# Kernel tuning notes

Hardware: AMD Instinct MI355X
Metric: run time of the kernel (lower is better)

## Reference

```python
import jax, jax.numpy as jnp
import numpy as np

T = 2048          # patch tokens (multiple of 128 -> flash padding is no-op)
D = 1280          # hidden_size
H = 16            # num_heads
HD = D // H       # 80 head_dim
HALF = HD // 2    # 40 rotary dim
FF = 3420         # intermediate_size
DEPTH = 4
MERGE = 4         # spatial_merge_size**2
OUT = 3584        # merger d_model
PATCH_IN = 1176   # 3*2*14*14
WIN = 64          # tokens per attention window
EPS = 1e-6
SCALE = 1.0 / float(np.sqrt(HD))


def setup_inputs() -> dict:
    key = jax.random.key(0)
    ks = iter(jax.random.split(key, 64))
    rn = lambda shape, s=0.02: jax.random.normal(next(ks), shape, jnp.float32) * s
    inp = {}
    inp["x"] = jax.random.normal(next(ks), (T, PATCH_IN), jnp.float32)
    inp["rotary_pos_emb"] = jax.random.uniform(next(ks), (T, HALF), jnp.float32) * 6.2832
    inp["cu_window_seqlens"] = jnp.arange(0, T + 1, WIN, dtype=jnp.int32)  # [33]
    inp["patch_w"] = rn((PATCH_IN, D))
    # per-block params, stacked on leading DEPTH axis for lax.scan
    inp["qkv_w"] = rn((DEPTH, D, 3 * D))
    inp["qkv_b"] = rn((DEPTH, 3 * D))
    inp["proj_w"] = rn((DEPTH, D, D))
    inp["proj_b"] = rn((DEPTH, D))
    inp["norm1_s"] = jnp.ones((DEPTH, D), jnp.float32)
    inp["norm2_s"] = jnp.ones((DEPTH, D), jnp.float32)
    inp["gate_w"] = rn((DEPTH, D, FF))
    inp["gate_b"] = rn((DEPTH, FF))
    inp["up_w"] = rn((DEPTH, D, FF))
    inp["up_b"] = rn((DEPTH, FF))
    inp["down_w"] = rn((DEPTH, FF, D))
    inp["down_b"] = rn((DEPTH, D))
    # patch merger
    inp["lnq_s"] = jnp.ones((D,), jnp.float32)
    inp["fc1_w"] = rn((MERGE * D, MERGE * D))
    inp["fc1_b"] = rn((MERGE * D,))
    inp["fc2_w"] = rn((MERGE * D, OUT))
    inp["fc2_b"] = rn((OUT,))
    return inp


def _rmsnorm(x, scale):
    return x * scale * jax.lax.rsqrt(jnp.mean(x * x, axis=-1, keepdims=True) + EPS)


def reference(x, rotary_pos_emb, cu_window_seqlens, patch_w, qkv_w, qkv_b,
              proj_w, proj_b, norm1_s, norm2_s, gate_w, gate_b, up_w, up_b,
              down_w, down_b, lnq_s, fc1_w, fc1_b, fc2_w, fc2_b):
    # patch embed: strided conv with kernel==stride is a plain matmul
    h = x @ patch_w  # [T, D]

    # windowed segment ids (generate_window_segment_ids); T % 128 == 0 -> no pad
    idx = jnp.arange(T, dtype=jnp.int32)
    seg = jnp.searchsorted(cu_window_seqlens[1:], idx, side='right') + 1
    mask = seg[:, None] == seg[None, :]  # [T, T] window attention mask

    cos = jnp.cos(rotary_pos_emb)  # [T, HALF]
    sin = jnp.sin(rotary_pos_emb)

    def rope(t):  # t: [T, H, HD]
        r, i = t[..., :HALF], t[..., HALF:]
        c, s = cos[:, None, :], sin[:, None, :]
        return jnp.concatenate([r * c - i * s, r * s + i * c], axis=-1)

    def block(h, p):
        qw, qb, pw, pb, n1, n2, gw, gb, uw, ub, dw, db = p
        n = _rmsnorm(h, n1)
        q, k, v = jnp.split(n @ qw + qb, 3, axis=-1)
        q = rope(q.reshape(T, H, HD))
        k = rope(k.reshape(T, H, HD))
        v = v.reshape(T, H, HD)
        scores = jnp.einsum('qhd,khd->hqk', q, k) * SCALE
        scores = jnp.where(mask[None], scores, -1e30)
        attn = jax.nn.softmax(scores, axis=-1)
        o = jnp.einsum('hqk,khd->qhd', attn, v).reshape(T, D)
        h = h + o @ pw + pb
        n = _rmsnorm(h, n2)
        h = h + (jax.nn.silu(n @ gw + gb) * (n @ uw + ub)) @ dw + db
        return h, None

    h, _ = jax.lax.scan(block, h, (qkv_w, qkv_b, proj_w, proj_b, norm1_s,
                                   norm2_s, gate_w, gate_b, up_w, up_b,
                                   down_w, down_b))

    # patch merger: RMSNorm -> merge 2x2 spatial patches -> MLP
    m = _rmsnorm(h, lnq_s).reshape(-1, MERGE * D)  # [T//4, 5120]
    m = jax.nn.gelu(m @ fc1_w + fc1_b, approximate=False)
    return m @ fc2_w + fc2_b  # [T//4, OUT]
```

## Files before the change

### kernel.cpp

```cpp
#include <hip/hip_runtime.h>
#include <hip/hip_bf16.h>
#include <cstdint>
#include <cstddef>
#include <math.h>

#define T_TOK 2048
#define DMODEL 1280
#define NHEAD 16
#define HDIM 80
#define HALFD 40
#define FFDIM 3420
#define FF_PAD 3456
#define FFK_PAD 3424
#define PATCH_INDIM 1176
#define PATCHK_PAD 1184
#define DEPTH_L 4
#define OUTD 3584
#define WIN 64
#define NWIN (T_TOK / WIN)
#define MERGED 5120
#define EPSV 1e-6f
#define SCALE_ATTN 0.11180339887498949f

typedef __attribute__((ext_vector_type(8))) short short8;
typedef __attribute__((ext_vector_type(4))) float f32x4;
typedef unsigned short ushort_t;

template<int BN>
__global__ __launch_bounds__(256) void gemm_bf16(
    const ushort_t* __restrict__ A, const ushort_t* __restrict__ Bt,
    const float* __restrict__ bias, const float* __restrict__ res,
    float* __restrict__ C, int M, int Nreal, int Nc, int Kp)
{
    constexpr int MI = (BN == 128) ? 4 : 2;
    __shared__ ushort_t As[3][128 * 32];
    __shared__ ushort_t Bs[3][BN * 32];

    const int tid  = threadIdx.x;
    const int lane = tid & 63;
    const int wave = tid >> 6;

    const int row0 = blockIdx.y * 128;
    const int col0 = blockIdx.x * BN;
    const int wm0  = (BN == 128) ? (wave & 1) * 64 : wave * 32;
    const int wn0  = (BN == 128) ? (wave >> 1) * 64 : 0;

    f32x4 acc[MI][4] = {};

    const int ldr = tid >> 2;
    const int ldc = ((tid & 3) ^ (ldr & 3)) * 8;

    const int mrow = lane & 15;
    const int kswz = ((lane >> 4) ^ (mrow & 3)) * 8;
    const int nt   = Kp >> 5;

    auto stage = [&](int buf, int kk) {
        const ushort_t* ga = A  + (size_t)(row0 + ldr) * Kp + kk + ldc;
        __builtin_amdgcn_global_load_lds(
            (const __attribute__((address_space(1))) void*)ga,
            (__attribute__((address_space(3))) void*)(&As[buf][tid * 8]), 16, 0, 0);
        __builtin_amdgcn_global_load_lds(
            (const __attribute__((address_space(1))) void*)(ga + (size_t)64 * Kp),
            (__attribute__((address_space(3))) void*)(&As[buf][2048 + tid * 8]), 16, 0, 0);
        const ushort_t* gb = Bt + (size_t)(col0 + ldr) * Kp + kk + ldc;
        __builtin_amdgcn_global_load_lds(
            (const __attribute__((address_space(1))) void*)gb,
            (__attribute__((address_space(3))) void*)(&Bs[buf][tid * 8]), 16, 0, 0);
        if constexpr (BN == 128) {
            __builtin_amdgcn_global_load_lds(
                (const __attribute__((address_space(1))) void*)(gb + (size_t)64 * Kp),
                (__attribute__((address_space(3))) void*)(&Bs[buf][2048 + tid * 8]), 16, 0, 0);
        }
    };

    stage(0, 0);
    if (nt > 1) stage(1, 32);

    int cur = 0;
    for (int t = 0; t < nt; ++t) {
        if (t + 1 < nt) {
            if constexpr (BN == 128) asm volatile("s_waitcnt vmcnt(4)" ::: "memory");
            else                     asm volatile("s_waitcnt vmcnt(3)" ::: "memory");
        } else {
            asm volatile("s_waitcnt vmcnt(0)" ::: "memory");
        }
        __builtin_amdgcn_s_barrier();

        short8 af[MI], bf[4];
        #pragma unroll
        for (int i = 0; i < MI; i++)
            af[i] = *(const short8*)&As[cur][(wm0 + i * 16 + mrow) * 32 + kswz];
        #pragma unroll
        for (int j = 0; j < 4; j++)
            bf[j] = *(const short8*)&Bs[cur][(wn0 + j * 16 + mrow) * 32 + kswz];

        __builtin_amdgcn_s_setprio(1);
        #pragma unroll
        for (int i = 0; i < MI; i++)
            #pragma unroll
            for (int j = 0; j < 4; j++)
                acc[i][j] = __builtin_amdgcn_mfma_f32_16x16x32_bf16(
                    af[i], bf[j], acc[i][j], 0, 0, 0);
        __builtin_amdgcn_s_setprio(0);

        if (t + 2 < nt) {
            int pf = cur + 2; if (pf >= 3) pf -= 3;
            stage(pf, (t + 2) * 32);
        }
        cur = (cur == 2) ? 0 : cur + 1;
    }

    const int crow0 = row0 + wm0 + (lane >> 4) * 4;
    const int ccol0 = col0 + wn0 + (lane & 15);
    #pragma unroll
    for (int j = 0; j < 4; j++) {
        const int col = ccol0 + j * 16;
        if (col >= Nreal) continue;
        const float bv = bias ? bias[col] : 0.f;
        #pragma unroll
        for (int i = 0; i < MI; i++) {
            #pragma unroll
            for (int r = 0; r < 4; r++) {
                const int row = crow0 + i * 16 + r;
                float v = acc[i][j][r] + bv;
                if (res) v += res[(size_t)row * Nc + col];
                C[(size_t)row * Nc + col] = v;
            }
        }
    }
}

__global__ __launch_bounds__(256) void transpose_cvt(
    const float* __restrict__ in, __hip_bfloat16* __restrict__ out,
    int K, int N, int Kp, int Np)
{
    __shared__ float t[32][33];
    const int k0 = blockIdx.x * 32, n0 = blockIdx.y * 32;
    const int tx = threadIdx.x & 31, ty = threadIdx.x >> 5;
    #pragma unroll
    for (int i = 0; i < 4; i++) {
        const int k = k0 + ty + i * 8, n = n0 + tx;
        t[ty + i * 8][tx] = (k < K && n < N) ? in[(size_t)k * N + n] : 0.f;
    }
    __syncthreads();
    #pragma unroll
    for (int i = 0; i < 4; i++) {
        const int n = n0 + ty + i * 8, k = k0 + tx;
        if (n < Np && k < Kp)
            out[(size_t)n * Kp + k] = __float2bfloat16(t[tx][ty + i * 8]);
    }
}

__global__ __launch_bounds__(256) void cvt_pad(
    const float* __restrict__ in, __hip_bfloat16* __restrict__ out,
    int M, int K, int Kp)
{
    const int i = blockIdx.x * 256 + threadIdx.x;
    if (i >= M * Kp) return;
    const int m = i / Kp, k = i - m * Kp;
    out[i] = __float2bfloat16(k < K ? in[(size_t)m * K + k] : 0.f);
}

__global__ __launch_bounds__(256) void rmsnorm_kernel(
    const float* __restrict__ x, const float* __restrict__ scale,
    __hip_bfloat16* __restrict__ out, int D)
{
    const int row = blockIdx.x;
    const float* xr = x + (size_t)row * D;
    float ss = 0.f;
    for (int i = threadIdx.x; i < D; i += 256) { const float v = xr[i]; ss += v * v; }
    for (int off = 32; off > 0; off >>= 1) ss += __shfl_down(ss, off);
    __shared__ float red[4];
    if ((threadIdx.x & 63) == 0) red[threadIdx.x >> 6] = ss;
    __syncthreads();
    const float tot = red[0] + red[1] + red[2] + red[3];
    const float inv = rsqrtf(tot / (float)D + EPSV);
    __hip_bfloat16* orow = out + (size_t)row * D;
    for (int i = threadIdx.x; i < D; i += 256)
        orow[i] = __float2bfloat16(xr[i] * scale[i] * inv);
}

__global__ __launch_bounds__(256) void rope_kernel(
    float* __restrict__ qkv, const float* __restrict__ rpe)
{
    const int i = blockIdx.x * 256 + threadIdx.x;
    if (i >= T_TOK * NHEAD * HALFD) return;
    const int t = i / (NHEAD * HALFD);
    const int rem = i - t * (NHEAD * HALFD);
    const int hh = rem / HALFD;
    const int j = rem - hh * HALFD;
    const float ang = rpe[t * HALFD + j];
    const float c = cosf(ang), s = sinf(ang);
    const size_t qb = (size_t)t * (3 * DMODEL) + hh * HDIM + j;
    float r = qkv[qb], im = qkv[qb + HALFD];
    qkv[qb] = r * c - im * s;
    qkv[qb + HALFD] = r * s + im * c;
    const size_t kb = qb + DMODEL;
    r = qkv[kb]; im = qkv[kb + HALFD];
    qkv[kb] = r * c - im * s;
    qkv[kb + HALFD] = r * s + im * c;
}

__global__ __launch_bounds__(256) void attn_kernel(
    const float* __restrict__ qkv, __hip_bfloat16* __restrict__ o)
{
    __shared__ float qs[WIN][HDIM + 1];
    __shared__ float ks[WIN][HDIM + 1];
    __shared__ float ps[WIN][WIN];
    const int win = blockIdx.x, hh = blockIdx.y;
    const int t0 = win * WIN;
    const int tid = threadIdx.x;

    for (int i = tid; i < WIN * HDIM; i += 256) {
        const int r = i / HDIM, d = i - r * HDIM;
        const size_t base = (size_t)(t0 + r) * (3 * DMODEL) + hh * HDIM + d;
        qs[r][d] = qkv[base];
        ks[r][d] = qkv[base + DMODEL];
    }
    __syncthreads();

    const int row = tid >> 2, sub = tid & 3;
    float s[16];
    #pragma unroll
    for (int jj = 0; jj < 16; jj++) s[jj] = 0.f;
    for (int d = 0; d < HDIM; d++) {
        const float qv = qs[row][d];
        #pragma unroll
        for (int jj = 0; jj < 16; jj++) s[jj] += qv * ks[sub * 16 + jj][d];
    }
    float mx = -1e30f;
    #pragma unroll
    for (int jj = 0; jj < 16; jj++) { s[jj] *= SCALE_ATTN; mx = fmaxf(mx, s[jj]); }
    for (int off = 1; off < 4; off <<= 1) mx = fmaxf(mx, __shfl_xor(mx, off));
    float l = 0.f;
    #pragma unroll
    for (int jj = 0; jj < 16; jj++) { s[jj] = expf(s[jj] - mx); l += s[jj]; }
    for (int off = 1; off < 4; off <<= 1) l += __shfl_xor(l, off);
    const float inv = 1.f / l;
    #pragma unroll
    for (int jj = 0; jj < 16; jj++) ps[row][sub * 16 + jj] = s[jj] * inv;
    __syncthreads();

    for (int i = tid; i < WIN * HDIM; i += 256) {
        const int r = i / HDIM, d = i - r * HDIM;
        ks[r][d] = qkv[(size_t)(t0 + r) * (3 * DMODEL) + 2 * DMODEL + hh * HDIM + d];
    }
    __syncthreads();

    for (int i = tid; i < WIN * HDIM; i += 256) {
        const int r = i / HDIM, d = i - r * HDIM;
        float acc = 0.f;
        #pragma unroll
        for (int j = 0; j < WIN; j++) acc += ps[r][j] * ks[j][d];
        o[(size_t)(t0 + r) * DMODEL + hh * HDIM + d] = __float2bfloat16(acc);
    }
}

__global__ __launch_bounds__(256) void silumul_kernel(
    const float* __restrict__ g, const float* __restrict__ u,
    __hip_bfloat16* __restrict__ out)
{
    const int i = blockIdx.x * 256 + threadIdx.x;
    if (i >= T_TOK * FFK_PAD) return;
    const int row = i / FFK_PAD, k = i - row * FFK_PAD;
    float v = 0.f;
    if (k < FFDIM) {
        const float x = g[(size_t)row * FF_PAD + k];
        v = (x / (1.f + expf(-x))) * u[(size_t)row * FF_PAD + k];
    }
    out[i] = __float2bfloat16(v);
}

__global__ __launch_bounds__(256) void gelu_kernel(
    const float* __restrict__ x, __hip_bfloat16* __restrict__ out, int n)
{
    const int i = blockIdx.x * 256 + threadIdx.x;
    if (i < n) {
        const float v = x[i];
        out[i] = __float2bfloat16(0.5f * v * (1.f + erff(v * 0.70710678118654752f)));
    }
}

extern "C" void kernel_launch(void* const* d_in, const int* in_sizes, int n_in,
                              void* d_out, int out_size, void* d_ws, size_t ws_size,
                              hipStream_t stream)
{
    const float* x       = (const float*)d_in[0];
    const float* rpe     = (const float*)d_in[1];
    const float* patch_w = (const float*)d_in[3];
    const float* qkv_w   = (const float*)d_in[4];
    const float* qkv_b   = (const float*)d_in[5];
    const float* proj_w  = (const float*)d_in[6];
    const float* proj_b  = (const float*)d_in[7];
    const float* norm1_s = (const float*)d_in[8];
    const float* norm2_s = (const float*)d_in[9];
    const float* gate_w  = (const float*)d_in[10];
    const float* gate_b  = (const float*)d_in[11];
    const float* up_w    = (const float*)d_in[12];
    const float* up_b    = (const float*)d_in[13];
    const float* down_w  = (const float*)d_in[14];
    const float* down_b  = (const float*)d_in[15];
    const float* lnq_s   = (const float*)d_in[16];
    const float* fc1_w   = (const float*)d_in[17];
    const float* fc1_b   = (const float*)d_in[18];
    const float* fc2_w   = (const float*)d_in[19];
    const float* fc2_b   = (const float*)d_in[20];
    float* out = (float*)d_out;

    char* p = (char*)d_ws;
    auto alloc = [&](size_t bytes) -> void* {
        void* r = (void*)p; p += (bytes + 255) & ~(size_t)255; return r;
    };
    float* h    = (float*)alloc((size_t)T_TOK * DMODEL * 4);
    float* qkvf = (float*)alloc((size_t)T_TOK * 3 * DMODEL * 4);
    float* gf   = (float*)alloc((size_t)T_TOK * FF_PAD * 4);
    float* uf   = (float*)alloc((size_t)T_TOK * FF_PAD * 4);
    float* fc1f = (float*)alloc((size_t)512 * MERGED * 4);
    __hip_bfloat16* x_b    = (__hip_bfloat16*)alloc((size_t)T_TOK * PATCHK_PAD * 2);
    __hip_bfloat16* n_b    = (__hip_bfloat16*)alloc((size_t)T_TOK * DMODEL * 2);
    __hip_bfloat16* o_b    = (__hip_bfloat16*)alloc((size_t)T_TOK * DMODEL * 2);
    __hip_bfloat16* g_b    = (__hip_bfloat16*)alloc((size_t)T_TOK * FFK_PAD * 2);
    __hip_bfloat16* m_b    = (__hip_bfloat16*)alloc((size_t)512 * MERGED * 2);
    __hip_bfloat16* patch_t= (__hip_bfloat16*)alloc((size_t)DMODEL * PATCHK_PAD * 2);
    __hip_bfloat16* qkv_t  = (__hip_bfloat16*)alloc((size_t)3 * DMODEL * DMODEL * 2);
    __hip_bfloat16* proj_t = (__hip_bfloat16*)alloc((size_t)DMODEL * DMODEL * 2);
    __hip_bfloat16* gate_t = (__hip_bfloat16*)alloc((size_t)FF_PAD * DMODEL * 2);
    __hip_bfloat16* up_t   = (__hip_bfloat16*)alloc((size_t)FF_PAD * DMODEL * 2);
    __hip_bfloat16* down_t = (__hip_bfloat16*)alloc((size_t)DMODEL * FFK_PAD * 2);
    __hip_bfloat16* fc1_t  = (__hip_bfloat16*)alloc((size_t)MERGED * MERGED * 2);
    __hip_bfloat16* fc2_t  = (__hip_bfloat16*)alloc((size_t)OUTD * MERGED * 2);

    const dim3 blk(256);
    auto gemm = [&](const __hip_bfloat16* A, const __hip_bfloat16* Bt,
                    const float* bias, const float* res, float* C,
                    int M, int Nreal, int Nc, int Kp, int bn) {
        if (bn == 64) {
            dim3 grid(Nc / 64, M / 128);
            gemm_bf16<64><<<grid, blk, 0, stream>>>((const ushort_t*)A, (const ushort_t*)Bt,
                                                    bias, res, C, M, Nreal, Nc, Kp);
        } else {
            dim3 grid(Nc / 128, M / 128);
            gemm_bf16<128><<<grid, blk, 0, stream>>>((const ushort_t*)A, (const ushort_t*)Bt,
                                                     bias, res, C, M, Nreal, Nc, Kp);
        }
    };
    auto tcvt = [&](const float* in, __hip_bfloat16* o2, int K, int N, int Kp, int Np) {
        dim3 grid((Kp + 31) / 32, (Np + 31) / 32);
        transpose_cvt<<<grid, blk, 0, stream>>>(in, o2, K, N, Kp, Np);
    };

    cvt_pad<<<(T_TOK * PATCHK_PAD + 255) / 256, blk, 0, stream>>>(
        x, x_b, T_TOK, PATCH_INDIM, PATCHK_PAD);
    tcvt(patch_w, patch_t, PATCH_INDIM, DMODEL, PATCHK_PAD, DMODEL);
    tcvt(fc1_w, fc1_t, MERGED, MERGED, MERGED, MERGED);
    tcvt(fc2_w, fc2_t, MERGED, OUTD, MERGED, OUTD);

    gemm(x_b, patch_t, nullptr, nullptr, h, T_TOK, DMODEL, DMODEL, PATCHK_PAD, 64);

    for (int l = 0; l < DEPTH_L; l++) {
        tcvt(qkv_w + (size_t)l * DMODEL * 3 * DMODEL, qkv_t, DMODEL, 3 * DMODEL,
             DMODEL, 3 * DMODEL);
        tcvt(proj_w + (size_t)l * DMODEL * DMODEL, proj_t, DMODEL, DMODEL,
             DMODEL, DMODEL);
        tcvt(gate_w + (size_t)l * DMODEL * FFDIM, gate_t, DMODEL, FFDIM,
             DMODEL, FF_PAD);
        tcvt(up_w + (size_t)l * DMODEL * FFDIM, up_t, DMODEL, FFDIM,
             DMODEL, FF_PAD);
        tcvt(down_w + (size_t)l * FFDIM * DMODEL, down_t, FFDIM, DMODEL,
             FFK_PAD, DMODEL);

        rmsnorm_kernel<<<T_TOK, blk, 0, stream>>>(h, norm1_s + l * DMODEL, n_b, DMODEL);
        gemm(n_b, qkv_t, qkv_b + l * 3 * DMODEL, nullptr, qkvf,
             T_TOK, 3 * DMODEL, 3 * DMODEL, DMODEL, 64);
        rope_kernel<<<(T_TOK * NHEAD * HALFD + 255) / 256, blk, 0, stream>>>(qkvf, rpe);
        attn_kernel<<<dim3(NWIN, NHEAD), blk, 0, stream>>>(qkvf, o_b);
        gemm(o_b, proj_t, proj_b + l * DMODEL, h, h, T_TOK, DMODEL, DMODEL, DMODEL, 64);

        rmsnorm_kernel<<<T_TOK, blk, 0, stream>>>(h, norm2_s + l * DMODEL, n_b, DMODEL);
        gemm(n_b, gate_t, gate_b + l * FFDIM, nullptr, gf,
             T_TOK, FFDIM, FF_PAD, DMODEL, 64);
        gemm(n_b, up_t, up_b + l * FFDIM, nullptr, uf,
             T_TOK, FFDIM, FF_PAD, DMODEL, 64);
        silumul_kernel<<<(T_TOK * FFK_PAD + 255) / 256, blk, 0, stream>>>(gf, uf, g_b);
        gemm(g_b, down_t, down_b + l * DMODEL, h, h, T_TOK, DMODEL, DMODEL, FFK_PAD, 64);
    }

    rmsnorm_kernel<<<T_TOK, blk, 0, stream>>>(h, lnq_s, n_b, DMODEL);
    gemm(n_b, fc1_t, fc1_b, nullptr, fc1f, 512, MERGED, MERGED, MERGED, 128);
    gelu_kernel<<<(512 * MERGED + 255) / 256, blk, 0, stream>>>(fc1f, m_b, 512 * MERGED);
    gemm(m_b, fc2_t, fc2_b, nullptr, out, 512, OUTD, OUTD, MERGED, 128);
}
```

Baseline: 2.030 ms.

## Add split-K GEMM with reduction kernels, fuse gate/up GEMMs, use 128-wide tiles

Adds split-K support to the bf16 GEMM through gridDim.z. Each z-slice writes fp32 partials, and new reduction kernels sum them while applying bias and residual, with GELU fused into the fc1 reduction. The gate and up weights are packed into one matrix so a single GEMM produces both, and their biases are applied in the SiLU-mul kernel. All GEMMs now use the 128x128 tile, aimed at better CU occupancy on the narrow-N and small-M GEMMs. The cost is extra partial-buffer traffic and more kernel launches.

```diff
diff --git a/kernel.cpp b/kernel.cpp
--- a/kernel.cpp
+++ b/kernel.cpp
@@ -11,6 +11,7 @@
 #define HALFD 40
 #define FFDIM 3420
 #define FF_PAD 3456
+#define GU_N (2 * FF_PAD)
 #define FFK_PAD 3424
 #define PATCH_INDIM 1176
 #define PATCHK_PAD 1184
@@ -52,7 +53,13 @@
 
     const int mrow = lane & 15;
     const int kswz = ((lane >> 4) ^ (mrow & 3)) * 8;
-    const int nt   = Kp >> 5;
+
+    const int nt_all = Kp >> 5;
+    const int S   = gridDim.z;
+    const int per = (nt_all + S - 1) / S;
+    const int tA  = blockIdx.z * per;
+    const int tE  = (tA + per < nt_all) ? (tA + per) : nt_all;
+    const int cnt = tE - tA;
 
     auto stage = [&](int buf, int kk) {
         const ushort_t* ga = A  + (size_t)(row0 + ldr) * Kp + kk + ldc;
@@ -73,60 +80,112 @@
         }
     };
 
-    stage(0, 0);
-    if (nt > 1) stage(1, 32);
-
-    int cur = 0;
-    for (int t = 0; t < nt; ++t) {
-        if (t + 1 < nt) {
-            if constexpr (BN == 128) asm volatile("s_waitcnt vmcnt(4)" ::: "memory");
-            else                     asm volatile("s_waitcnt vmcnt(3)" ::: "memory");
-        } else {
-            asm volatile("s_waitcnt vmcnt(0)" ::: "memory");
-        }
-        __builtin_amdgcn_s_barrier();
-
-        short8 af[MI], bf[4];
-        #pragma unroll
-        for (int i = 0; i < MI; i++)
-            af[i] = *(const short8*)&As[cur][(wm0 + i * 16 + mrow) * 32 + kswz];
-        #pragma unroll
-        for (int j = 0; j < 4; j++)
-            bf[j] = *(const short8*)&Bs[cur][(wn0 + j * 16 + mrow) * 32 + kswz];
-
-        __builtin_amdgcn_s_setprio(1);
-        #pragma unroll
-        for (int i = 0; i < MI; i++)
+    if (cnt > 0) {
+        stage(0, tA * 32);
+        if (cnt > 1) stage(1, (tA + 1) * 32);
+
+        int cur = 0;
+        for (int t = 0; t < cnt; ++t) {
+            if (t + 1 < cnt) {
+                if constexpr (BN == 128) asm volatile("s_waitcnt vmcnt(4)" ::: "memory");
+                else                     asm volatile("s_waitcnt vmcnt(3)" ::: "memory");
+            } else {
+                asm volatile("s_waitcnt vmcnt(0)" ::: "memory");
+            }
+            __builtin_amdgcn_s_barrier();
+
+            short8 af[MI], bf[4];
+            #pragma unroll
+            for (int i = 0; i < MI; i++)
+                af[i] = *(const short8*)&As[cur][(wm0 + i * 16 + mrow) * 32 + kswz];
             #pragma unroll
             for (int j = 0; j < 4; j++)
-                acc[i][j] = __builtin_amdgcn_mfma_f32_16x16x32_bf16(
-                    af[i], bf[j], acc[i][j], 0, 0, 0);
-        __builtin_amdgcn_s_setprio(0);
-
-        if (t + 2 < nt) {
-            int pf = cur + 2; if (pf >= 3) pf -= 3;
-            stage(pf, (t + 2) * 32);
+                bf[j] = *(const short8*)&Bs[cur][(wn0 + j * 16 + mrow) * 32 + kswz];
+
+            __builtin_amdgcn_s_setprio(1);
+            #pragma unroll
+            for (int i = 0; i < MI; i++)
+                #pragma unroll
+                for (int j = 0; j < 4; j++)
+                    acc[i][j] = __builtin_amdgcn_mfma_f32_16x16x32_bf16(
+                        af[i], bf[j], acc[i][j], 0, 0, 0);
+            __builtin_amdgcn_s_setprio(0);
+
+            if (t + 2 < cnt) {
+                int pf = cur + 2; if (pf >= 3) pf -= 3;
+                stage(pf, (tA + t + 2) * 32);
+            }
+            cur = (cur == 2) ? 0 : cur + 1;
         }
-        cur = (cur == 2) ? 0 : cur + 1;
     }
 
     const int crow0 = row0 + wm0 + (lane >> 4) * 4;
     const int ccol0 = col0 + wn0 + (lane & 15);
-    #pragma unroll
-    for (int j = 0; j < 4; j++) {
-        const int col = ccol0 + j * 16;
-        if (col >= Nreal) continue;
-        const float bv = bias ? bias[col] : 0.f;
+    if (gridDim.z > 1) {
+        float* Cz = C + (size_t)blockIdx.z * ((size_t)M * Nc);
         #pragma unroll
-        for (int i = 0; i < MI; i++) {
+        for (int j = 0; j < 4; j++) {
+            const int col = ccol0 + j * 16;
             #pragma unroll
-            for (int r = 0; r < 4; r++) {
-                const int row = crow0 + i * 16 + r;
-                float v = acc[i][j][r] + bv;
-                if (res) v += res[(size_t)row * Nc + col];
-                C[(size_t)row * Nc + col] = v;
+            for (int i = 0; i < MI; i++)
+                #pragma unroll
+                for (int r = 0; r < 4; r++)
+                    Cz[(size_t)(crow0 + i * 16 + r) * Nc + col] = acc[i][j][r];
+        }
+    } else {
+        #pragma unroll
+        for (int j = 0; j < 4; j++) {
+            const int col = ccol0 + j * 16;
+            if (col >= Nreal) continue;
+            const float bv = bias ? bias[col] : 0.f;
+            #pragma unroll
+            for (int i = 0; i < MI; i++) {
+                #pragma unroll
+                for (int r = 0; r < 4; r++) {
+                    const int row = crow0 + i * 16 + r;
+                    float v = acc[i][j][r] + bv;
+                    if (res) v += res[(size_t)row * Nc + col];
+                    C[(size_t)row * Nc + col] = v;
+                }
             }
         }
+    }
+}
+
+__global__ __launch_bounds__(256) void reduce_sum(
+    const float* __restrict__ p, const float* __restrict__ bias,
+    const float* __restrict__ res, float* __restrict__ out,
+    int len4, int Nc, int S)
+{
+    const int i = blockIdx.x * 256 + threadIdx.x;
+    if (i >= len4) return;
+    const size_t e = (size_t)i * 4;
+    const int col = (int)(e % (size_t)Nc);
+    f32x4 acc = {0.f, 0.f, 0.f, 0.f};
+    if (bias) acc += *(const f32x4*)&bias[col];
+    if (res)  acc += *(const f32x4*)&res[e];
+    const size_t stride = (size_t)len4 * 4;
+    for (int z = 0; z < S; z++)
+        acc += *(const f32x4*)&p[(size_t)z * stride + e];
+    *(f32x4*)&out[e] = acc;
+}
+
+__global__ __launch_bounds__(256) void reduce_gelu_bf16(
+    const float* __restrict__ p, const float* __restrict__ bias,
+    __hip_bfloat16* __restrict__ out, int len4, int Nc, int S)
+{
+    const int i = blockIdx.x * 256 + threadIdx.x;
+    if (i >= len4) return;
+    const size_t e = (size_t)i * 4;
+    const int col = (int)(e % (size_t)Nc);
+    f32x4 acc = *(const f32x4*)&bias[col];
+    const size_t stride = (size_t)len4 * 4;
+    for (int z = 0; z < S; z++)
+        acc += *(const f32x4*)&p[(size_t)z * stride + e];
+    #pragma unroll
+    for (int q = 0; q < 4; q++) {
+        const float v = acc[q];
+        out[e + q] = __float2bfloat16(0.5f * v * (1.f + erff(v * 0.70710678118654752f)));
     }
 }
 
@@ -257,28 +316,19 @@
 }
 
 __global__ __launch_bounds__(256) void silumul_kernel(
-    const float* __restrict__ g, const float* __restrict__ u,
-    __hip_bfloat16* __restrict__ out)
+    const float* __restrict__ gu, const float* __restrict__ gb,
+    const float* __restrict__ ub, __hip_bfloat16* __restrict__ out)
 {
     const int i = blockIdx.x * 256 + threadIdx.x;
     if (i >= T_TOK * FFK_PAD) return;
     const int row = i / FFK_PAD, k = i - row * FFK_PAD;
     float v = 0.f;
     if (k < FFDIM) {
-        const float x = g[(size_t)row * FF_PAD + k];
-        v = (x / (1.f + expf(-x))) * u[(size_t)row * FF_PAD + k];
+        const float g = gu[(size_t)row * GU_N + k] + gb[k];
+        const float u = gu[(size_t)row * GU_N + FF_PAD + k] + ub[k];
+        v = (g / (1.f + expf(-g))) * u;
     }
     out[i] = __float2bfloat16(v);
-}
-
-__global__ __launch_bounds__(256) void gelu_kernel(
-    const float* __restrict__ x, __hip_bfloat16* __restrict__ out, int n)
-{
-    const int i = blockIdx.x * 256 + threadIdx.x;
-    if (i < n) {
-        const float v = x[i];
-        out[i] = __float2bfloat16(0.5f * v * (1.f + erff(v * 0.70710678118654752f)));
-    }
 }
 
 extern "C" void kernel_launch(void* const* d_in, const int* in_sizes, int n_in,
@@ -313,9 +363,8 @@
     };
     float* h    = (float*)alloc((size_t)T_TOK * DMODEL * 4);
     float* qkvf = (float*)alloc((size_t)T_TOK * 3 * DMODEL * 4);
-    float* gf   = (float*)alloc((size_t)T_TOK * FF_PAD * 4);
-    float* uf   = (float*)alloc((size_t)T_TOK * FF_PAD * 4);
-    float* fc1f = (float*)alloc((size_t)512 * MERGED * 4);
+    float* guf  = (float*)alloc((size_t)T_TOK * GU_N * 4);
+    float* pbuf = (float*)alloc((size_t)4 * T_TOK * DMODEL * 4);
     __hip_bfloat16* x_b    = (__hip_bfloat16*)alloc((size_t)T_TOK * PATCHK_PAD * 2);
     __hip_bfloat16* n_b    = (__hip_bfloat16*)alloc((size_t)T_TOK * DMODEL * 2);
     __hip_bfloat16* o_b    = (__hip_bfloat16*)alloc((size_t)T_TOK * DMODEL * 2);
@@ -324,8 +373,7 @@
     __hip_bfloat16* patch_t= (__hip_bfloat16*)alloc((size_t)DMODEL * PATCHK_PAD * 2);
     __hip_bfloat16* qkv_t  = (__hip_bfloat16*)alloc((size_t)3 * DMODEL * DMODEL * 2);
     __hip_bfloat16* proj_t = (__hip_bfloat16*)alloc((size_t)DMODEL * DMODEL * 2);
-    __hip_bfloat16* gate_t = (__hip_bfloat16*)alloc((size_t)FF_PAD * DMODEL * 2);
-    __hip_bfloat16* up_t   = (__hip_bfloat16*)alloc((size_t)FF_PAD * DMODEL * 2);
+    __hip_bfloat16* gu_t   = (__hip_bfloat16*)alloc((size_t)GU_N * DMODEL * 2);
     __hip_bfloat16* down_t = (__hip_bfloat16*)alloc((size_t)DMODEL * FFK_PAD * 2);
     __hip_bfloat16* fc1_t  = (__hip_bfloat16*)alloc((size_t)MERGED * MERGED * 2);
     __hip_bfloat16* fc2_t  = (__hip_bfloat16*)alloc((size_t)OUTD * MERGED * 2);
@@ -333,21 +381,20 @@
     const dim3 blk(256);
     auto gemm = [&](const __hip_bfloat16* A, const __hip_bfloat16* Bt,
                     const float* bias, const float* res, float* C,
-                    int M, int Nreal, int Nc, int Kp, int bn) {
-        if (bn == 64) {
-            dim3 grid(Nc / 64, M / 128);
-            gemm_bf16<64><<<grid, blk, 0, stream>>>((const ushort_t*)A, (const ushort_t*)Bt,
-                                                    bias, res, C, M, Nreal, Nc, Kp);
-        } else {
-            dim3 grid(Nc / 128, M / 128);
-            gemm_bf16<128><<<grid, blk, 0, stream>>>((const ushort_t*)A, (const ushort_t*)Bt,
-                                                     bias, res, C, M, Nreal, Nc, Kp);
-        }
+                    int M, int Nreal, int Nc, int Kp, int S) {
+        dim3 grid(Nc / 128, M / 128, S);
+        gemm_bf16<128><<<grid, blk, 0, stream>>>((const ushort_t*)A, (const ushort_t*)Bt,
+                                                 bias, res, C, M, Nreal, Nc, Kp);
     };
     auto tcvt = [&](const float* in, __hip_bfloat16* o2, int K, int N, int Kp, int Np) {
         dim3 grid((Kp + 31) / 32, (Np + 31) / 32);
         transpose_cvt<<<grid, blk, 0, stream>>>(in, o2, K, N, Kp, Np);
     };
+    auto redsum = [&](const float* pp, const float* bias, const float* res,
+                      float* o2, int len, int Nc, int S) {
+        const int len4 = len / 4;
+        reduce_sum<<<(len4 + 255) / 256, blk, 0, stream>>>(pp, bias, res, o2, len4, Nc, S);
+    };
 
     cvt_pad<<<(T_TOK * PATCHK_PAD + 255) / 256, blk, 0, stream>>>(
         x, x_b, T_TOK, PATCH_INDIM, PATCHK_PAD);
@@ -355,38 +402,44 @@
     tcvt(fc1_w, fc1_t, MERGED, MERGED, MERGED, MERGED);
     tcvt(fc2_w, fc2_t, MERGED, OUTD, MERGED, OUTD);
 
-    gemm(x_b, patch_t, nullptr, nullptr, h, T_TOK, DMODEL, DMODEL, PATCHK_PAD, 64);
+    gemm(x_b, patch_t, nullptr, nullptr, pbuf, T_TOK, DMODEL, DMODEL, PATCHK_PAD, 2);
+    redsum(pbuf, nullptr, nullptr, h, T_TOK * DMODEL, DMODEL, 2);
 
     for (int l = 0; l < DEPTH_L; l++) {
         tcvt(qkv_w + (size_t)l * DMODEL * 3 * DMODEL, qkv_t, DMODEL, 3 * DMODEL,
              DMODEL, 3 * DMODEL);
         tcvt(proj_w + (size_t)l * DMODEL * DMODEL, proj_t, DMODEL, DMODEL,
              DMODEL, DMODEL);
-        tcvt(gate_w + (size_t)l * DMODEL * FFDIM, gate_t, DMODEL, FFDIM,
+        tcvt(gate_w + (size_t)l * DMODEL * FFDIM, gu_t, DMODEL, FFDIM,
              DMODEL, FF_PAD);
-        tcvt(up_w + (size_t)l * DMODEL * FFDIM, up_t, DMODEL, FFDIM,
-             DMODEL, FF_PAD);
+        tcvt(up_w + (size_t)l * DMODEL * FFDIM, gu_t + (size_t)FF_PAD * DMODEL,
+             DMODEL, FFDIM, DMODEL, FF_PAD);
         tcvt(down_w + (size_t)l * FFDIM * DMODEL, down_t, FFDIM, DMODEL,
              FFK_PAD, DMODEL);
 
         rmsnorm_kernel<<<T_TOK, blk, 0, stream>>>(h, norm1_s + l * DMODEL, n_b, DMODEL);
         gemm(n_b, qkv_t, qkv_b + l * 3 * DMODEL, nullptr, qkvf,
-             T_TOK, 3 * DMODEL, 3 * DMODEL, DMODEL, 64);
+             T_TOK, 3 * DMODEL, 3 * DMODEL, DMODEL, 1);
         rope_kernel<<<(T_TOK * NHEAD * HALFD + 255) / 256, blk, 0, stream>>>(qkvf, rpe);
         attn_kernel<<<dim3(NWIN, NHEAD), blk, 0, stream>>>(qkvf, o_b);
-        gemm(o_b, proj_t, proj_b + l * DMODEL, h, h, T_TOK, DMODEL, DMODEL, DMODEL, 64);
+        gemm(o_b, proj_t, nullptr, nullptr, pbuf, T_TOK, DMODEL, DMODEL, DMODEL, 4);
+        redsum(pbuf, proj_b + l * DMODEL, h, h, T_TOK * DMODEL, DMODEL, 4);
 
         rmsnorm_kernel<<<T_TOK, blk, 0, stream>>>(h, norm2_s + l * DMODEL, n_b, DMODEL);
-        gemm(n_b, gate_t, gate_b + l * FFDIM, nullptr, gf,
-             T_TOK, FFDIM, FF_PAD, DMODEL, 64);
-        gemm(n_b, up_t, up_b + l * FFDIM, nullptr, uf,
-             T_TOK, FFDIM, FF_PAD, DMODEL, 64);
-        silumul_kernel<<<(T_TOK * FFK_PAD + 255) / 256, blk, 0, stream>>>(gf, uf, g_b);
-        gemm(g_b, down_t, down_b + l * DMODEL, h, h, T_TOK, DMODEL, DMODEL, FFK_PAD, 64);
+        gemm(n_b, gu_t, nullptr, nullptr, guf, T_TOK, GU_N, GU_N, DMODEL, 1);
+        silumul_kernel<<<(T_TOK * FFK_PAD + 255) / 256, blk, 0, stream>>>(
+            guf, gate_b + l * FFDIM, up_b + l * FFDIM, g_b);
+        gemm(g_b, down_t, nullptr, nullptr, pbuf, T_TOK, DMODEL, DMODEL, FFK_PAD, 4);
+        redsum(pbuf, down_b + l * DMODEL, h, h, T_TOK * DMODEL, DMODEL, 4);
     }
 
     rmsnorm_kernel<<<T_TOK, blk, 0, stream>>>(h, lnq_s, n_b, DMODEL);
-    gemm(n_b, fc1_t, fc1_b, nullptr, fc1f, 512, MERGED, MERGED, MERGED, 128);
-    gelu_kernel<<<(512 * MERGED + 255) / 256, blk, 0, stream>>>(fc1f, m_b, 512 * MERGED);
-    gemm(m_b, fc2_t, fc2_b, nullptr, out, 512, OUTD, OUTD, MERGED, 128);
-}
+    gemm(n_b, fc1_t, nullptr, nullptr, pbuf, 512, MERGED, MERGED, MERGED, 4);
+    {
+        const int len4 = (512 * MERGED) / 4;
+        reduce_gelu_bf16<<<(len4 + 255) / 256, blk, 0, stream>>>(
+            pbuf, fc1_b, m_b, len4, MERGED, 4);
+    }
+    gemm(m_b, fc2_t, nullptr, nullptr, pbuf, 512, OUTD, OUTD, MERGED, 4);
+    redsum(pbuf, fc2_b, nullptr, out, 512 * OUTD, OUTD, 4);
+}
```

Result: faster. 1.819 ms (-10.4%).
